# Optimization experiments

Measured on AMD Instinct MI355X. Metric: run time of the kernel, lower is better.

## Reference

```python
import jax, jax.numpy as jnp
import numpy as np

EPS = 1e-12  # torch F.normalize clamp epsilon
NOISE = np.array([1e-05, 2e-05, 3e-05], dtype=np.float32)  # diagonal regularizer


def setup_inputs() -> dict:
    key = jax.random.key(0)
    B, C = 65536, 128
    v_feat = jax.random.normal(key, (B, C, 3), dtype=jnp.float32)
    return {"v_feat": v_feat}


def reference(v_feat):
    # L2 normalize each 3-vector (B, C, 3) along last dim
    norm = jnp.sqrt(jnp.sum(v_feat * v_feat, axis=-1, keepdims=True))
    v = v_feat / jnp.maximum(norm, EPS)

    # Covariance M = v^T v  -> (B, 3, 3), plus tiny diagonal noise for stability
    M = jnp.einsum('bci,bcj->bij', v, v) + jnp.diag(jnp.asarray(NOISE))[None, :, :]

    # Batched symmetric 3x3 eigendecomposition (ascending eigenvalues)
    _, evecs = jnp.linalg.eigh(M)  # evecs: (B, 3, 3), columns are eigenvectors
    v1 = evecs[:, :, 0]  # (B, 3)
    v2 = evecs[:, :, 1]

    # Sign disambiguation: align with the mean direction of the features
    def fix_sign(vec):
        s = jnp.sign(jnp.sum(v * vec[:, None, :], axis=(1, 2)))  # (B,)
        s = jnp.where(s == 0, 1.0, s)
        return vec * s[:, None]

    v1 = fix_sign(v1)
    v2 = fix_sign(v2)
    v3 = jnp.cross(v1, v2)

    # Frame: columns [v1 v2 v3] -> (B, 3, 3)
    return jnp.stack([v1, v2, v3], axis=-1)
```

## Files before the change

### kernel.cpp

```cpp
#include <hip/hip_runtime.h>
#include <math.h>
#include <stdint.h>


#define BLOCK 256
#define BPB   64
#define NIT   4

template <int CTRL>
__device__ __forceinline__ float ror16_f32(float v) {
    union { float f; int i; } u, r;
    u.f = v;
    r.i = __builtin_amdgcn_mov_dpp(u.i, CTRL, 0xF, 0xF, true);
    return r.f;
}

__device__ __forceinline__ float frsqrt(float x) {
    float r = __builtin_amdgcn_rsqf(x);
    return r * fmaf(-0.5f * x, r * r, 1.5f);
}
__device__ __forceinline__ float frcp(float x) {
    float r = __builtin_amdgcn_rcpf(x);
    return r * fmaf(-x, r, 2.0f);
}

template <int P, int Q, int R>
__device__ __forceinline__ void jrot(float (&A)[3][3], float (&V)[3][3]) {
    float apq = A[P][Q];
    if (fabsf(apq) > 1e-12f) {
        float theta = (A[Q][Q] - A[P][P]) * 0.5f * frcp(apq);
        float q = fmaf(theta, theta, 1.0f);
        float sq = q * frsqrt(q);
        float t = frcp(fabsf(theta) + sq);
        if (theta < 0.0f) t = -t;
        float c = frsqrt(fmaf(t, t, 1.0f));
        float s = t * c;
        float apq_t = t * apq;
        A[P][P] = A[P][P] - apq_t;
        A[Q][Q] = A[Q][Q] + apq_t;
        A[P][Q] = 0.0f;
        A[Q][P] = 0.0f;
        float apr = A[P][R], aqr = A[Q][R];
        A[P][R] = fmaf(c, apr, -s * aqr); A[R][P] = A[P][R];
        A[Q][R] = fmaf(s, apr,  c * aqr); A[R][Q] = A[Q][R];
#pragma unroll
        for (int i = 0; i < 3; ++i) {
            float vip = V[i][P], viq = V[i][Q];
            V[i][P] = fmaf(c, vip, -s * viq);
            V[i][Q] = fmaf(s, vip,  c * viq);
        }
    }
}

__device__ __forceinline__ void accum8(const float4 (&q)[6], float (&m)[8]) {
    float f[24];
#pragma unroll
    for (int i = 0; i < 6; ++i) {
        f[4 * i + 0] = q[i].x; f[4 * i + 1] = q[i].y;
        f[4 * i + 2] = q[i].z; f[4 * i + 3] = q[i].w;
    }
#pragma unroll
    for (int k = 0; k < 8; ++k) {
        float fx = f[3 * k + 0];
        float fy = f[3 * k + 1];
        float fz = f[3 * k + 2];
        float n2 = fmaf(fx, fx, fmaf(fy, fy, fz * fz));
        float inv = __builtin_amdgcn_rsqf(fmaxf(n2, 1e-24f));
        float x = fx * inv;
        float y = fy * inv;
        float z = fz * inv;
        m[0] = fmaf(x, x, m[0]);
        m[1] = fmaf(x, y, m[1]);
        m[2] = fmaf(x, z, m[2]);
        m[3] = fmaf(y, y, m[3]);
        m[4] = fmaf(y, z, m[4]);
        m[5] += x; m[6] += y; m[7] += z;
    }
}

__device__ __forceinline__ void reduce16(float (&m)[8]) {
#pragma unroll
    for (int k = 0; k < 8; ++k) m[k] += ror16_f32<0x121>(m[k]);
#pragma unroll
    for (int k = 0; k < 8; ++k) m[k] += ror16_f32<0x122>(m[k]);
#pragma unroll
    for (int k = 0; k < 8; ++k) m[k] += ror16_f32<0x124>(m[k]);
#pragma unroll
    for (int k = 0; k < 8; ++k) m[k] += ror16_f32<0x128>(m[k]);
}

__global__ __launch_bounds__(BLOCK) void vn_fused(
    const float* __restrict__ vf, float* __restrict__ out, int B) {
    __shared__ __align__(16) float sA[BPB][9];

    const int tid  = threadIdx.x;
    const int wave = tid >> 6;
    const int lane = tid & 63;
    const int g    = lane >> 4;
    const int sub  = lane & 15;

    const int blockBase = blockIdx.x * BPB;
    const int slot0 = wave * (4 * NIT) + g;

    auto loadq = [&](int b, float4 (&q)[6]) {
        const float4* p =
            reinterpret_cast<const float4*>(vf + (size_t)b * 384 + sub * 24);
#pragma unroll
        for (int i = 0; i < 6; ++i) q[i] = p[i];
    };

    float4 q0[6], q1[6];
    {
        const int b0 = blockBase + slot0;
        if (b0 < B) loadq(b0, q0);
    }

#pragma unroll
    for (int it = 0; it < NIT; ++it) {
        float4 (&qc)[6] = (it & 1) ? q1 : q0;
        float4 (&qn)[6] = (it & 1) ? q0 : q1;
        const int slot = slot0 + it * 4;
        const int b = blockBase + slot;
        if (it + 1 < NIT) {
            const int bn = b + 4;
            if (bn < B) loadq(bn, qn);
        }
        if (b < B) {
            float m[8];
#pragma unroll
            for (int k = 0; k < 8; ++k) m[k] = 0.0f;
            accum8(qc, m);
            reduce16(m);
            if (sub == 0) {
#pragma unroll
                for (int k = 0; k < 8; ++k) sA[slot][k] = m[k];
            }
        }
    }

    __syncthreads();

    if (tid < BPB) {
        const int b = blockBase + tid;
        if (b < B) {
            float m[8];
#pragma unroll
            for (int k = 0; k < 8; ++k) m[k] = sA[tid][k];

            float A[3][3], V[3][3];
            A[0][0] = m[0] + 1e-05f;
            A[0][1] = m[1]; A[1][0] = m[1];
            A[0][2] = m[2]; A[2][0] = m[2];
            A[1][1] = m[3] + 2e-05f;
            A[1][2] = m[4]; A[2][1] = m[4];
            A[2][2] = (128.0f - m[0] - m[3]) + 3e-05f;
#pragma unroll
            for (int i = 0; i < 3; ++i)
#pragma unroll
                for (int j = 0; j < 3; ++j) V[i][j] = (i == j) ? 1.0f : 0.0f;

#pragma unroll
            for (int sweep = 0; sweep < 4; ++sweep) {
                jrot<0, 1, 2>(A, V);
                jrot<0, 2, 1>(A, V);
                jrot<1, 2, 0>(A, V);
            }

            float e0 = A[0][0], e1 = A[1][1], e2 = A[2][2];
            float c0x = V[0][0], c0y = V[1][0], c0z = V[2][0];
            float c1x = V[0][1], c1y = V[1][1], c1z = V[2][1];
            float c2x = V[0][2], c2y = V[1][2], c2z = V[2][2];

#define CSWAP(ea, eb, ax, ay, az, bx, by, bz)                         \
            if (ea > eb) {                                            \
                float t_;                                             \
                t_ = ea; ea = eb; eb = t_;                            \
                t_ = ax; ax = bx; bx = t_;                            \
                t_ = ay; ay = by; by = t_;                            \
                t_ = az; az = bz; bz = t_;                            \
            }
            CSWAP(e0, e1, c0x, c0y, c0z, c1x, c1y, c1z)
            CSWAP(e1, e2, c1x, c1y, c1z, c2x, c2y, c2z)
            CSWAP(e0, e1, c0x, c0y, c0z, c1x, c1y, c1z)
#undef CSWAP

            float s0 = m[5], s1 = m[6], s2 = m[7];
            float d1 = s0 * c0x + s1 * c0y + s2 * c0z;
            float f1 = (d1 < 0.0f) ? -1.0f : 1.0f;
            c0x *= f1; c0y *= f1; c0z *= f1;
            float d2 = s0 * c1x + s1 * c1y + s2 * c1z;
            float f2 = (d2 < 0.0f) ? -1.0f : 1.0f;
            c1x *= f2; c1y *= f2; c1z *= f2;

            float v3x = c0y * c1z - c0z * c1y;
            float v3y = c0z * c1x - c0x * c1z;
            float v3z = c0x * c1y - c0y * c1x;

            sA[tid][0] = c0x; sA[tid][1] = c1x; sA[tid][2] = v3x;
            sA[tid][3] = c0y; sA[tid][4] = c1y; sA[tid][5] = v3y;
            sA[tid][6] = c0z; sA[tid][7] = c1z; sA[tid][8] = v3z;
        }
    }

    __syncthreads();

    if (blockBase + BPB <= B) {
        if (tid < (BPB * 9) / 4) {
            const float4* s4 = reinterpret_cast<const float4*>(&sA[0][0]);
            float4* o4 = reinterpret_cast<float4*>(out + (size_t)blockBase * 9);
            o4[tid] = s4[tid];
        }
    } else if (tid < BPB) {
        const int b = blockBase + tid;
        if (b < B) {
            float* o = out + (size_t)b * 9;
#pragma unroll
            for (int k = 0; k < 9; ++k) o[k] = sA[tid][k];
        }
    }
}

extern "C" void kernel_launch(void* const* d_in, const int* in_sizes, int n_in,
                              void* d_out, int out_size, void* d_ws, size_t ws_size,
                              hipStream_t stream) {
    const float* vf = (const float*)d_in[0];
    float* out = (float*)d_out;
    const int B = in_sizes[0] / 384;
    const int grid = (B + BPB - 1) / BPB;
    vn_fused<<<dim3(grid), dim3(BLOCK), 0, stream>>>(vf, out, B);
}
```

Before: 24.61 us.

## Stage input tiles into LDS via async global_load_lds with swizzled double buffering

Replaces per-thread register float4 loads with direct global-to-LDS async copies (global_load_lds) that are fully coalesced. A 16-batch tile is double-buffered and read back through an XOR swizzle to avoid bank conflicts. The aim is better coalescing and overlap of loads with compute, at the cost of extra LDS (about 48KB), a __syncthreads per tile, and possible occupancy loss. Correctness depends on the global-side swizzle matching the LDS read-side swizzle.

```diff
diff --git a/kernel.cpp b/kernel.cpp
--- a/kernel.cpp
+++ b/kernel.cpp
@@ -3,9 +3,14 @@
 #include <stdint.h>
 
 
-#define BLOCK 256
-#define BPB   64
-#define NIT   4
+#define BLOCK      256
+#define TILE_B     16
+#define TILE_QUADS (TILE_B * 96)
+#define NT         4
+#define BPB        (TILE_B * NT)
+#define NSTAGE     6
+
+__device__ __forceinline__ uint32_t swz(uint32_t q) { return q ^ ((q >> 3) & 7u); }
 
 template <int CTRL>
 __device__ __forceinline__ float ror16_f32(float v) {
@@ -52,13 +57,7 @@
     }
 }
 
-__device__ __forceinline__ void accum8(const float4 (&q)[6], float (&m)[8]) {
-    float f[24];
-#pragma unroll
-    for (int i = 0; i < 6; ++i) {
-        f[4 * i + 0] = q[i].x; f[4 * i + 1] = q[i].y;
-        f[4 * i + 2] = q[i].z; f[4 * i + 3] = q[i].w;
-    }
+__device__ __forceinline__ void accum8(const float (&f)[24], float (&m)[8]) {
 #pragma unroll
     for (int k = 0; k < 8; ++k) {
         float fx = f[3 * k + 0];
@@ -91,57 +90,69 @@
 
 __global__ __launch_bounds__(BLOCK) void vn_fused(
     const float* __restrict__ vf, float* __restrict__ out, int B) {
+    __shared__ __align__(16) float sbuf[2][TILE_QUADS * 4];
     __shared__ __align__(16) float sA[BPB][9];
 
     const int tid  = threadIdx.x;
     const int wave = tid >> 6;
     const int lane = tid & 63;
-    const int g    = lane >> 4;
-    const int sub  = lane & 15;
-
-    const int blockBase = blockIdx.x * BPB;
-    const int slot0 = wave * (4 * NIT) + g;
-
-    auto loadq = [&](int b, float4 (&q)[6]) {
-        const float4* p =
-            reinterpret_cast<const float4*>(vf + (size_t)b * 384 + sub * 24);
-#pragma unroll
-        for (int i = 0; i < 6; ++i) q[i] = p[i];
+    const uint32_t lswz = (uint32_t)lane ^ ((uint32_t)lane >> 3);
+
+    const size_t maxQuad = (size_t)B * 96;
+    const size_t tile0   = (size_t)blockIdx.x * NT;
+
+    auto stage = [&](int bufi, int t) {
+#pragma unroll
+        for (int i = 0; i < NSTAGE; ++i) {
+            const uint32_t rowQuad = (uint32_t)(i * 4 + wave) * 64;
+            size_t gq = (tile0 + (size_t)t) * TILE_QUADS + rowQuad + lswz;
+            if (gq >= maxQuad) gq = maxQuad - 1;
+            const float* gsrc = vf + gq * 4;
+            float* ldst = &sbuf[bufi][((size_t)rowQuad + (uint32_t)lane) * 4];
+            __builtin_amdgcn_global_load_lds(
+                (__attribute__((address_space(1))) void*)(void*)const_cast<float*>(gsrc),
+                (__attribute__((address_space(3))) void*)(void*)ldst,
+                16, 0, 0);
+        }
     };
 
-    float4 q0[6], q1[6];
-    {
-        const int b0 = blockBase + slot0;
-        if (b0 < B) loadq(b0, q0);
-    }
-
-#pragma unroll
-    for (int it = 0; it < NIT; ++it) {
-        float4 (&qc)[6] = (it & 1) ? q1 : q0;
-        float4 (&qn)[6] = (it & 1) ? q0 : q1;
-        const int slot = slot0 + it * 4;
-        const int b = blockBase + slot;
-        if (it + 1 < NIT) {
-            const int bn = b + 4;
-            if (bn < B) loadq(bn, qn);
-        }
-        if (b < B) {
-            float m[8];
-#pragma unroll
-            for (int k = 0; k < 8; ++k) m[k] = 0.0f;
-            accum8(qc, m);
-            reduce16(m);
-            if (sub == 0) {
-#pragma unroll
-                for (int k = 0; k < 8; ++k) sA[slot][k] = m[k];
-            }
-        }
-    }
-
+    stage(0, 0);
     __syncthreads();
 
+    const int g   = lane >> 4;
+    const int sub = lane & 15;
+    const int slotInTile = wave * 4 + g;
+
+    for (int t = 0; t < NT; ++t) {
+        if (t + 1 < NT) stage((t + 1) & 1, t + 1);
+        const float* buf = sbuf[t & 1];
+
+        const uint32_t baseQuad = (uint32_t)slotInTile * 96 + (uint32_t)sub * 6;
+        float f[24];
+#pragma unroll
+        for (int j = 0; j < 6; ++j) {
+            const uint32_t pq = swz(baseQuad + (uint32_t)j);
+            const float4 q = *reinterpret_cast<const float4*>(&buf[pq * 4]);
+            f[4 * j + 0] = q.x; f[4 * j + 1] = q.y;
+            f[4 * j + 2] = q.z; f[4 * j + 3] = q.w;
+        }
+
+        float m[8];
+#pragma unroll
+        for (int k = 0; k < 8; ++k) m[k] = 0.0f;
+        accum8(f, m);
+        reduce16(m);
+
+        if (sub == 0) {
+            const int slot = t * TILE_B + slotInTile;
+#pragma unroll
+            for (int k = 0; k < 8; ++k) sA[slot][k] = m[k];
+        }
+        __syncthreads();
+    }
+
     if (tid < BPB) {
-        const int b = blockBase + tid;
+        const int b = blockIdx.x * BPB + tid;
         if (b < B) {
             float m[8];
 #pragma unroll
@@ -204,6 +215,7 @@
 
     __syncthreads();
 
+    const int blockBase = blockIdx.x * BPB;
     if (blockBase + BPB <= B) {
         if (tid < (BPB * 9) / 4) {
             const float4* s4 = reinterpret_cast<const float4*>(&sA[0][0]);
```

Result: slower. 26.08 us (+6.0%).
